# Performance work log

Measured on AMD Instinct MI355X. Metric: run time of the kernel, lower is better.

## Reference

```python
import math
import jax, jax.numpy as jnp
import numpy as np

NHEAD = 4
EPS = 1e-5


def make_pe(max_len, d):
    pos = np.arange(max_len, dtype=np.float32)[:, None]
    div = np.exp(np.arange(0, d, 2, dtype=np.float32) * (-math.log(10000.0) / d))
    pe = np.zeros((max_len, d), np.float32)
    pe[:, 0::2] = np.sin(pos * div)
    pe[:, 1::2] = np.cos(pos * div)
    return jnp.asarray(pe)


def layer_norm(x, g, b):
    m = jnp.mean(x, axis=-1, keepdims=True)
    v = jnp.mean((x - m) ** 2, axis=-1, keepdims=True)
    return (x - m) / jnp.sqrt(v + EPS) * g + b


def mha(q, k, v, wq, bq, wk, bk, wv, bv, wo, bo, kmask=None):
    # q: [b, Lq, d], k/v: [b, Lk, d]
    b_, lq, d = q.shape
    lk = k.shape[1]
    hd = d // NHEAD
    qh = (q @ wq + bq).reshape(b_, lq, NHEAD, hd)
    kh = (k @ wk + bk).reshape(b_, lk, NHEAD, hd)
    vh = (v @ wv + bv).reshape(b_, lk, NHEAD, hd)
    s = jnp.einsum('bqhd,bkhd->bhqk', qh, kh) / jnp.sqrt(jnp.float32(hd))
    if kmask is not None:
        s = jnp.where(kmask[None, None, None, :], s, jnp.float32(-1e9))
    a = jax.nn.softmax(s, axis=-1)
    o = jnp.einsum('bhqk,bkhd->bqhd', a, vh).reshape(b_, lq, d)
    return o @ wo + bo


def _forward(src, in_w, in_b, dec_start,
             e_wq, e_bq, e_wk, e_bk, e_wv, e_bv, e_wo, e_bo,
             e_ln1_g, e_ln1_b, e_w1, e_b1, e_w2, e_b2, e_ln2_g, e_ln2_b,
             d_swq, d_sbq, d_swk, d_sbk, d_swv, d_sbv, d_swo, d_sbo,
             d_ln1_g, d_ln1_b,
             d_cwq, d_cbq, d_cwk, d_cbk, d_cwv, d_cbv, d_cwo, d_cbo,
             d_ln2_g, d_ln2_b,
             d_w1, d_b1, d_w2, d_b2, d_ln3_g, d_ln3_b,
             out_w, out_b, tgt_len):
    B, S = src.shape
    d = in_w.shape[1]
    T = tgt_len
    pe = make_pe(max(S, T) + 10, d)

    # ---- encoder (1 post-norm layer, relu FFN, dropout off) ----
    x = (src[..., None] @ in_w + in_b) * jnp.sqrt(jnp.float32(d))  # [B,S,d]
    x = x + pe[None, :S]
    x = layer_norm(x + mha(x, x, x, e_wq, e_bq, e_wk, e_bk, e_wv, e_bv, e_wo, e_bo), e_ln1_g, e_ln1_b)
    mem = layer_norm(x + (jax.nn.relu(x @ e_w1 + e_b1) @ e_w2 + e_b2), e_ln2_g, e_ln2_b)

    buf0 = jnp.zeros((B, T + 1, d), src.dtype).at[:, 0].set(dec_start[0, 0])
    pe_dec = pe[None, :T + 1]
    kidx = jnp.arange(T + 1)

    def step(buf, t):
        di = buf + pe_dec
        kmask = kidx <= t  # full (non-causal) attention over the t+1 valid tokens
        h = layer_norm(di + mha(di, di, di, d_swq, d_sbq, d_swk, d_sbk,
                                d_swv, d_sbv, d_swo, d_sbo, kmask=kmask),
                       d_ln1_g, d_ln1_b)
        h = layer_norm(h + mha(h, mem, mem, d_cwq, d_cbq, d_cwk, d_cbk,
                               d_cwv, d_cbv, d_cwo, d_cbo),
                       d_ln2_g, d_ln2_b)
        h = layer_norm(h + (jax.nn.relu(h @ d_w1 + d_b1) @ d_w2 + d_b2),
                       d_ln3_g, d_ln3_b)
        last = h[:, t]                       # [B,d] output at the newest position
        buf = buf.at[:, t + 1].set(last)     # feed back as next decoder token
        y = (last @ out_w + out_b)[:, 0]     # [B]
        return buf, y

    _, outs = jax.lax.scan(step, buf0, jnp.arange(T))  # outs: [T,B]
    return outs.T  # [B,T]


def setup_inputs():
    B, S, T, d, ff = 128, 512, 64, 48, 128
    ks = iter(jax.random.split(jax.random.key(0), 64))

    def w(shape, s=0.08):
        return jax.random.normal(next(ks), shape, jnp.float32) * s

    ones = lambda: jnp.ones((d,), jnp.float32)
    zeros = lambda: jnp.zeros((d,), jnp.float32)
    return dict(
        src=jax.random.normal(next(ks), (B, S), jnp.float32),
        in_w=w((1, d)), in_b=w((d,)),
        dec_start=w((1, 1, d), 1.0),
        e_wq=w((d, d)), e_bq=w((d,)), e_wk=w((d, d)), e_bk=w((d,)),
        e_wv=w((d, d)), e_bv=w((d,)), e_wo=w((d, d)), e_bo=w((d,)),
        e_ln1_g=ones(), e_ln1_b=zeros(),
        e_w1=w((d, ff)), e_b1=w((ff,)), e_w2=w((ff, d)), e_b2=w((d,)),
        e_ln2_g=ones(), e_ln2_b=zeros(),
        d_swq=w((d, d)), d_sbq=w((d,)), d_swk=w((d, d)), d_sbk=w((d,)),
        d_swv=w((d, d)), d_sbv=w((d,)), d_swo=w((d, d)), d_sbo=w((d,)),
        d_ln1_g=ones(), d_ln1_b=zeros(),
        d_cwq=w((d, d)), d_cbq=w((d,)), d_cwk=w((d, d)), d_cbk=w((d,)),
        d_cwv=w((d, d)), d_cbv=w((d,)), d_cwo=w((d, d)), d_cbo=w((d,)),
        d_ln2_g=ones(), d_ln2_b=zeros(),
        d_w1=w((d, ff)), d_b1=w((ff,)), d_w2=w((ff, d)), d_b2=w((d,)),
        d_ln3_g=ones(), d_ln3_b=zeros(),
        out_w=w((d, 1)), out_b=w((1,)),
        tgt_len=T,
    )


def reference(src, in_w, in_b, dec_start,
              e_wq, e_bq, e_wk, e_bk, e_wv, e_bv, e_wo, e_bo,
              e_ln1_g, e_ln1_b, e_w1, e_b1, e_w2, e_b2, e_ln2_g, e_ln2_b,
              d_swq, d_sbq, d_swk, d_sbk, d_swv, d_sbv, d_swo, d_sbo,
              d_ln1_g, d_ln1_b,
              d_cwq, d_cbq, d_cwk, d_cbk, d_cwv, d_cbv, d_cwo, d_cbo,
              d_ln2_g, d_ln2_b,
              d_w1, d_b1, d_w2, d_b2, d_ln3_g, d_ln3_b,
              out_w, out_b, tgt_len):
    return _forward(src, in_w, in_b, dec_start,
                    e_wq, e_bq, e_wk, e_bk, e_wv, e_bv, e_wo, e_bo,
                    e_ln1_g, e_ln1_b, e_w1, e_b1, e_w2, e_b2, e_ln2_g, e_ln2_b,
                    d_swq, d_sbq, d_swk, d_sbk, d_swv, d_sbv, d_swo, d_sbo,
                    d_ln1_g, d_ln1_b,
                    d_cwq, d_cbq, d_cwk, d_cbk, d_cwv, d_cbv, d_cwo, d_cbo,
                    d_ln2_g, d_ln2_b,
                    d_w1, d_b1, d_w2, d_b2, d_ln3_g, d_ln3_b,
                    out_w, out_b, tgt_len)
```

## Files before the change

### kernel.cpp

```cpp
#include <hip/hip_runtime.h>
#include <hip/hip_bf16.h>
#include <hip/hip_fp16.h>


constexpr int kB  = 128;
constexpr int kS  = 512;
constexpr int kT  = 64;
constexpr int kD  = 48;
constexpr int kFF = 128;
constexpr int kNH = 4;
constexpr int kHD = 12;

__device__ __forceinline__ void wsync(){
  __builtin_amdgcn_wave_barrier();
  asm volatile("" ::: "memory");
}

__device__ __forceinline__ float wsum(float v){
  #pragma unroll
  for(int o=32;o>=1;o>>=1) v += __shfl_xor(v,o,64);
  return v;
}
__device__ __forceinline__ float wmax(float v){
  #pragma unroll
  for(int o=32;o>=1;o>>=1) v = fmaxf(v,__shfl_xor(v,o,64));
  return v;
}

__device__ __forceinline__ float pe_val(int p, int j){
  int i = j >> 1;
  float f = expf(-0.19188209108283716f * (float)(2*i));
  float a = (float)p * f;
  return (j & 1) ? cosf(a) : sinf(a);
}
__device__ __forceinline__ float pe_fast(int p, int j){
  int i = j >> 1;
  float f = __expf(-0.19188209108283716f * (float)(2*i));
  float a = (float)p * f;
  return (j & 1) ? __cosf(a) : __sinf(a);
}

typedef _Float16 h2v __attribute__((ext_vector_type(2)));
union H2U { __half2 h; h2v v; };
__device__ __forceinline__ float fdot2(__half2 a, __half2 b, float c){
#if __has_builtin(__builtin_amdgcn_fdot2)
  H2U ua, ub; ua.h=a; ub.h=b;
  return __builtin_amdgcn_fdot2(ua.v, ub.v, c, false);
#else
  float2 fa=__half22float2(a), fb=__half22float2(b);
  return fmaf(fa.y, fb.y, fmaf(fa.x, fb.x, c));
#endif
}

__device__ __forceinline__ float dot48d(const __half2* x, const __half* w){
  const __half2* w2=(const __half2*)w;
  float a0=0.f,a1=0.f,a2=0.f,a3=0.f;
  #pragma unroll
  for(int c=0;c<6;c++){
    a0=fdot2(x[4*c+0],w2[4*c+0],a0);
    a1=fdot2(x[4*c+1],w2[4*c+1],a1);
    a2=fdot2(x[4*c+2],w2[4*c+2],a2);
    a3=fdot2(x[4*c+3],w2[4*c+3],a3);
  }
  return (a0+a1)+(a2+a3);
}
__device__ __forceinline__ float dot128d(const __half2* x, const __half* w){
  const __half2* w2=(const __half2*)w;
  float a0=0.f,a1=0.f,a2=0.f,a3=0.f,a4=0.f,a5=0.f,a6=0.f,a7=0.f;
  #pragma unroll
  for(int c=0;c<8;c++){
    a0=fdot2(x[8*c+0],w2[8*c+0],a0);
    a1=fdot2(x[8*c+1],w2[8*c+1],a1);
    a2=fdot2(x[8*c+2],w2[8*c+2],a2);
    a3=fdot2(x[8*c+3],w2[8*c+3],a3);
    a4=fdot2(x[8*c+4],w2[8*c+4],a4);
    a5=fdot2(x[8*c+5],w2[8*c+5],a5);
    a6=fdot2(x[8*c+6],w2[8*c+6],a6);
    a7=fdot2(x[8*c+7],w2[8*c+7],a7);
  }
  return ((a0+a1)+(a2+a3))+((a4+a5)+(a6+a7));
}
__device__ __forceinline__ float dot12f(const float4* x, const float4* k){
  float a=0.f;
  #pragma unroll
  for(int u=0;u<3;u++){ float4 xx=x[u], kk=k[u];
    a+=xx.x*kk.x+xx.y*kk.y+xx.z*kk.z+xx.w*kk.w; }
  return a;
}

__global__ void k_embed(const float* __restrict__ src, const float* __restrict__ in_w,
                        const float* __restrict__ in_b, float* __restrict__ X0){
  int idx = blockIdx.x*256 + threadIdx.x;
  if (idx >= kB*kS*kD) return;
  int j = idx % kD; int bs = idx / kD; int s = bs % kS;
  float v = (src[bs] * in_w[j] + in_b[j]) * 6.928203230275509f;
  X0[idx] = v + pe_fast(s, j);
}

__global__ void __launch_bounds__(256) k_qkv(const float* __restrict__ X,
    const float* __restrict__ wq, const float* __restrict__ bq,
    const float* __restrict__ wk, const float* __restrict__ bk,
    const float* __restrict__ wv, const float* __restrict__ bv,
    __half* __restrict__ Q, __half* __restrict__ K, __half* __restrict__ V){
  __shared__ __align__(16) __half W[3*2688];
  __shared__ __align__(16) float bias[3*kD];
  __shared__ __align__(16) __half2 xt2[32*24];
  int tid = threadIdx.x;
  for (int i=tid;i<3*2304;i+=256){ int m=i/2304, e=i%2304, k=e/48, j=e%48;
    const float* w = (m==0)?wq:((m==1)?wk:wv);
    W[m*2688 + j*56 + k] = __float2half(w[e]); }
  for (int i=tid;i<3*kD;i+=256){ int m=i/kD,e=i%kD;
    const float* w=(m==0)?bq:((m==1)?bk:bv); bias[i]=w[e]; }
  long row0 = (long)blockIdx.x*32;
  const float2* Xp=(const float2*)(X+row0*kD);
  for (int i=tid;i<768;i+=256){ float2 v=Xp[i]; xt2[i]=__floats2half2_rn(v.x,v.y); }
  __syncthreads();
  int r = tid>>3, c0 = tid&7;
  __half2 xr[24];
  #pragma unroll
  for(int u=0;u<24;u++) xr[u]=xt2[r*24+u];
  for (int c=c0; c<3*kD; c+=8){
    int m=c/kD, j=c%kD;
    float acc = bias[m*kD+j] + dot48d(xr, W + m*2688 + j*56);
    __half* o = (m==0)?Q:((m==1)?K:V);
    o[(row0+r)*kD+j]=__float2half(acc);
  }
}

__global__ void __launch_bounds__(256) k_attn(const __half* Q, const __half* __restrict__ K,
                       const __half* __restrict__ V, __half* O){
  int b = blockIdx.x / kNH, h = blockIdx.x % kNH;
  __shared__ __align__(16) __half2 Ks2[kS*6];
  __shared__ __align__(16) float   Vs[kS*kHD];
  int tid = threadIdx.x;
  long base = ((long)b*kS)*kD + h*kHD;
  for (int i=tid;i<kS*6;i+=256){ int r=i/6, c=i%6;
    Ks2[i]=*(const __half2*)&K[base+(long)r*kD+2*c]; }
  for (int i=tid;i<kS*kHD;i+=256){ int r=i/kHD, d=i%kHD;
    Vs[i]=__half2float(V[base+(long)r*kD+d]); }
  const float rs = 0.28867513459481287f;
  int q0 = tid, q1 = tid+256;
  __half2 qa2[6], qb2[6];
  {
    const __half2* qp0=(const __half2*)(Q+base+(long)q0*kD);
    const __half2* qp1=(const __half2*)(Q+base+(long)q1*kD);
    #pragma unroll
    for(int c=0;c<6;c++){ qa2[c]=qp0[c]; qb2[c]=qp1[c]; }
  }
  __syncthreads();
  float acc0[kHD], acc1[kHD];
  #pragma unroll
  for(int j=0;j<kHD;j++){ acc0[j]=0.f; acc1[j]=0.f; }
  float l0=0.f, l1=0.f;
  for(int k=0;k<kS;k++){
    const __half2* kp=Ks2+k*6;
    float sA0=0.f,sA1=0.f,sB0=0.f,sB1=0.f;
    #pragma unroll
    for(int c=0;c<3;c++){
      sA0=fdot2(qa2[2*c],kp[2*c],sA0); sA1=fdot2(qa2[2*c+1],kp[2*c+1],sA1);
      sB0=fdot2(qb2[2*c],kp[2*c],sB0); sB1=fdot2(qb2[2*c+1],kp[2*c+1],sB1);
    }
    float p0=__expf((sA0+sA1)*rs), p1=__expf((sB0+sB1)*rs);
    l0+=p0; l1+=p1;
    const float4* vp=(const float4*)(Vs+k*kHD);
    float4 va=vp[0], vb4=vp[1], vc4=vp[2];
    float vr[kHD]={va.x,va.y,va.z,va.w,vb4.x,vb4.y,vb4.z,vb4.w,vc4.x,vc4.y,vc4.z,vc4.w};
    #pragma unroll
    for(int j=0;j<kHD;j++){ acc0[j]+=p0*vr[j]; acc1[j]+=p1*vr[j]; }
  }
  float i0=1.f/l0, i1=1.f/l1;
  #pragma unroll
  for(int j=0;j<kHD;j++){
    O[base+(long)q0*kD+j]=__float2half(acc0[j]*i0);
    O[base+(long)q1*kD+j]=__float2half(acc1[j]*i1);
  }
}

__global__ void __launch_bounds__(256) k_oproj_ln(const float* __restrict__ Xres, const __half* __restrict__ O,
      const float* __restrict__ wo, const float* __restrict__ bo,
      const float* __restrict__ g, const float* __restrict__ bb,
      __half* __restrict__ Xout){
  __shared__ __align__(16) __half W[kD*56];
  __shared__ float bsh[kD], gs[kD], bs2[kD];
  __shared__ __align__(16) float res[32*kD];
  __shared__ __align__(16) __half2 ot2[32*24];
  __shared__ float mrow[32], rstd[32];
  int tid=threadIdx.x;
  for(int i=tid;i<kD*kD;i+=256){ int k=i/48, j=i%48; W[j*56+k]=__float2half(wo[i]); }
  if(tid<kD){ bsh[tid]=bo[tid]; gs[tid]=g[tid]; bs2[tid]=bb[tid]; }
  long row0=(long)blockIdx.x*32;
  const __half2* Op=(const __half2*)(O+row0*kD);
  for(int i=tid;i<768;i+=256) ot2[i]=Op[i];
  __syncthreads();
  int r=tid>>3, c0=tid&7;
  __half2 orow[24];
  #pragma unroll
  for(int u=0;u<24;u++) orow[u]=ot2[r*24+u];
  for(int j=c0;j<kD;j+=8){
    float acc=bsh[j]+dot48d(orow, W+j*56);
    res[r*kD+j]=Xres[row0*kD + r*kD + j]+acc;
  }
  __syncthreads();
  if(tid<32){
    float s=0.f, s2=0.f;
    for(int j=0;j<kD;j++){ float v=res[tid*kD+j]; s+=v; s2+=v*v; }
    float m=s*(1.f/kD);
    mrow[tid]=m; rstd[tid]=rsqrtf(s2*(1.f/kD)-m*m+1e-5f);
  }
  __syncthreads();
  for(int i=tid;i<32*kD;i+=256){int r2=i/kD,j=i%kD;
    Xout[row0*kD+i]=__float2half((res[i]-mrow[r2])*rstd[r2]*gs[j]+bs2[j]); }
}

__global__ void __launch_bounds__(256) k_ffn_ln(const __half* __restrict__ Xin,
   const float* __restrict__ w1, const float* __restrict__ b1,
   const float* __restrict__ w2, const float* __restrict__ b2,
   const float* __restrict__ g, const float* __restrict__ bb,
   float* __restrict__ Xout){
  __shared__ __align__(16) __half W1[kFF*56];
  __shared__ __align__(16) __half W2[kD*136];
  __shared__ float b1s[kFF], b2s[kD], gs[kD], bs2[kD];
  __shared__ __align__(16) __half xt[16*kD];
  __shared__ __align__(16) __half h1h[16*kFF];
  __shared__ __align__(16) float res[16*kD];
  __shared__ float mrow[16], rstd[16];
  int tid=threadIdx.x;
  for(int i=tid;i<kD*kFF;i+=256){ int k=i/128, c=i%128; W1[c*56+k]=__float2half(w1[i]); }
  for(int i=tid;i<kFF*kD;i+=256){ int u=i/48, j=i%48; W2[j*136+u]=__float2half(w2[i]); }
  if(tid<kFF) b1s[tid]=b1[tid];
  if(tid<kD){ b2s[tid]=b2[tid]; gs[tid]=g[tid]; bs2[tid]=bb[tid]; }
  long row0=(long)blockIdx.x*16;
  const __half2* Xp=(const __half2*)(Xin+row0*kD);
  for(int i=tid;i<384;i+=256) ((__half2*)xt)[i]=Xp[i];
  __syncthreads();
  int r=tid>>4, c0=tid&15;
  {
    __half2 xr[24];
    const __half2* xp=(const __half2*)(xt + r*kD);
    #pragma unroll
    for(int u=0;u<24;u++) xr[u]=xp[u];
    for(int c=c0;c<kFF;c+=16){
      float acc=b1s[c]+dot48d(xr, W1+c*56);
      h1h[r*kFF+c]=__float2half(fmaxf(acc,0.f));
    }
  }
  __syncthreads();
  {
    const __half2* hp=(const __half2*)(h1h + r*kFF);
    for(int j=c0;j<kD;j+=16){
      float acc=b2s[j]+dot128d(hp, W2+j*136);
      res[r*kD+j]=__half2float(xt[r*kD+j])+acc;
    }
  }
  __syncthreads();
  if(tid<16){
    float s=0.f, s2=0.f;
    for(int j=0;j<kD;j++){ float v=res[tid*kD+j]; s+=v; s2+=v*v; }
    float m=s*(1.f/kD);
    mrow[tid]=m; rstd[tid]=rsqrtf(s2*(1.f/kD)-m*m+1e-5f);
  }
  __syncthreads();
  for(int i=tid;i<16*kD;i+=256){int r2=i/kD,j=i%kD;
    Xout[row0*kD+i]=(res[i]-mrow[r2])*rstd[r2]*gs[j]+bs2[j]; }
}

__global__ void __launch_bounds__(256) k_ckv(const float* __restrict__ M,
    const float* __restrict__ wk, const float* __restrict__ bk,
    const float* __restrict__ wv, const float* __restrict__ bv,
    __half* __restrict__ Kc, __half* __restrict__ Vc){
  __shared__ __align__(16) __half W[2*2688];
  __shared__ float bias[2*kD];
  __shared__ __align__(16) __half2 xt2[32*24];
  int tid=threadIdx.x;
  for(int i=tid;i<2*2304;i+=256){ int m=i/2304, e=i%2304, k=e/48, j=e%48;
    W[m*2688 + j*56 + k] = __float2half((m?wv:wk)[e]); }
  for(int i=tid;i<2*kD;i+=256){ int m=i/kD,e=i%kD; bias[i]=(m?bv:bk)[e]; }
  long row0=(long)blockIdx.x*32;
  const float2* Mp=(const float2*)(M+row0*kD);
  for(int i=tid;i<768;i+=256){ float2 v=Mp[i]; xt2[i]=__floats2half2_rn(v.x,v.y); }
  __syncthreads();
  int r=tid>>3, c0=tid&7;
  __half2 xr[24];
  #pragma unroll
  for(int u=0;u<24;u++) xr[u]=xt2[r*24+u];
  long gr=row0+r; long bb2=gr>>9; long s=gr&511;
  for(int c=c0;c<2*kD;c+=8){
    int m=c/kD, j=c%kD;
    float acc=bias[m*kD+j]+dot48d(xr, W+m*2688+j*56);
    if(m==0) Kc[(bb2*kS+s)*kD + j]=__float2half(acc);
    else     Vc[(bb2*kD+j)*kS + s]=__float2half(acc);
  }
}

__global__ void k_prep(const float* __restrict__ swq,const float* __restrict__ swk,
                       const float* __restrict__ swv,const float* __restrict__ swo,
                       const float* __restrict__ cwq,const float* __restrict__ cwo,
                       const float* __restrict__ w1,const float* __restrict__ w2,
                       __half* __restrict__ Wh){
  int idx=blockIdx.x*256+threadIdx.x;
  if(idx>=26112) return;
  if(idx<13824){
    int m=idx/2304, e=idx%2304, j=e/48, k=e%48;
    const float* w = (m==0)?swq:((m==1)?swk:((m==2)?swv:((m==3)?swo:((m==4)?cwq:cwo))));
    Wh[m*2688 + j*56 + k] = __float2half(w[k*48+j]);
  } else if(idx<19968){
    int e=idx-13824, c=e/48, k=e%48;
    Wh[16128 + c*56 + k] = __float2half(w1[k*128+c]);
  } else {
    int e=idx-19968, j=e/128, u=e%128;
    Wh[23296 + j*136 + u] = __float2half(w2[u*48+j]);
  }
}

struct DecP {
  const float *dec_start, *sbq, *sbk, *sbv, *sbo, *ln1g, *ln1b,
              *cbq, *cbo, *ln2g, *ln2b, *fb1, *fb2, *ln3g, *ln3b, *ow, *ob;
};

__global__ void __launch_bounds__(256,1) k_dec(const __half* __restrict__ KT,
    const __half* __restrict__ VT, const __half* __restrict__ Wg, DecP P,
    float* __restrict__ out){
  __shared__ __align__(16) __half Wl[29824];
  __shared__ __align__(16) float Kh[kNH*kT*kHD];
  __shared__ __align__(16) float Vh[kNH*kT*kHD];
  __shared__ __align__(16) float qS[kNH*16];
  __shared__ __align__(16) __half xvH[kD], soH[kD], h1H[kD], cqH[kD], covH[kD], h2H[kD];
  __shared__ __align__(16) __half f1H[kFF];
  __shared__ __align__(16) float peT[kT*kD];
  int tid=threadIdx.x, b=blockIdx.x, wave=tid>>6, lane=tid&63;
  const float rs=0.28867513459481287f;

  for(int i=tid;i<29824/8;i+=256) ((float4*)Wl)[i]=((const float4*)Wg)[i];
  for(int i=tid;i<kT*kD;i+=256){ int tt=i/kD, j=i%kD; peT[i]=pe_val(tt,j); }

  float cur=0, c_bo=0,c_cbq=0,c_cbo=0,c_fb2=0;
  float g1=0,bb1=0,g2=0,bb2=0,g3=0,bb3=0,c_ow=0;
  if(wave==0 && lane<kD){
    cur=P.dec_start[lane];
    c_bo=P.sbo[lane]; c_cbq=P.cbq[lane]; c_cbo=P.cbo[lane]; c_fb2=P.fb2[lane];
    g1=P.ln1g[lane]; bb1=P.ln1b[lane];
    g2=P.ln2g[lane]; bb2=P.ln2b[lane];
    g3=P.ln3g[lane]; bb3=P.ln3b[lane];
    c_ow=P.ow[lane];
  }
  float c_qkvb=0;
  if(wave>=1 && lane<kD)
    c_qkvb = ((wave==1)?P.sbq:((wave==2)?P.sbk:P.sbv))[lane];
  float c_fb1=0;
  if(wave<2) c_fb1=P.fb1[wave*64+lane];
  float c_ob=P.ob[0];

  __half2 Kr2[4][2][6], Vr2[4][kHD];
  {
    const __half* Kb = KT + (long)b*kS*kD;
    const __half2* Vb = (const __half2*)VT + (long)b*kD*(kS/2);
    #pragma unroll
    for(int i=0;i<4;i++){
      int sp = lane + 64*i;
      #pragma unroll
      for(int e=0;e<2;e++){
        const __half2* kp=(const __half2*)(Kb + (long)(2*sp+e)*kD + wave*kHD);
        #pragma unroll
        for(int c=0;c<6;c++) Kr2[i][e][c]=kp[c];
      }
      #pragma unroll
      for(int u=0;u<kHD;u++) Vr2[i][u]=Vb[(wave*kHD+u)*(kS/2)+sp];
    }
  }
  __syncthreads();

  float h1=0, h2=0, xv=0;
  for(int t=0;t<kT;t++){
    if(wave==0 && lane<kD){ xv=cur+peT[t*kD+lane]; xvH[lane]=__float2half(xv); }
    __syncthreads();
    if(wave>=1 && lane<kD){
      int m=wave-1;
      float a=c_qkvb+dot48d((const __half2*)xvH, Wl + m*2688 + lane*56);
      int hh=lane/kHD, dd=lane%kHD;
      if(m==0) qS[hh*16+dd]=a;
      else if(m==1) Kh[(hh*kT+t)*kHD+dd]=a;
      else          Vh[(hh*kT+t)*kHD+dd]=a;
    }
    __syncthreads();
    {
      float p=0.f, pv[kHD];
      #pragma unroll
      for(int u=0;u<kHD;u++) pv[u]=0.f;
      if(lane<=t){
        float s=dot12f((const float4*)(qS+wave*16),
                       (const float4*)(Kh+(wave*kT+lane)*kHD))*rs;
        p=__expf(s);
        const float4* vp=(const float4*)(Vh+(wave*kT+lane)*kHD);
        float4 v0=vp[0], v1=vp[1], v2=vp[2];
        float vr[kHD]={v0.x,v0.y,v0.z,v0.w,v1.x,v1.y,v1.z,v1.w,v2.x,v2.y,v2.z,v2.w};
        #pragma unroll
        for(int u=0;u<kHD;u++) pv[u]=p*vr[u];
      }
      float l=wsum(p);
      #pragma unroll
      for(int u=0;u<kHD;u++) pv[u]=wsum(pv[u]);
      if(lane==0){
        float inv=1.f/l;
        #pragma unroll
        for(int u=0;u<6;u++)
          ((__half2*)soH)[wave*6+u]=__floats2half2_rn(pv[2*u]*inv, pv[2*u+1]*inv);
      }
    }
    __syncthreads();
    if(wave==0){
      float rr=0.f;
      if(lane<kD)
        rr=xv+c_bo+dot48d((const __half2*)soH, Wl+8064+lane*56);
      float s1=wsum(rr), s2=wsum(rr*rr);
      float mean=s1*(1.f/48.f);
      float rstd=rsqrtf(s2*(1.f/48.f)-mean*mean+1e-5f);
      h1=0;
      if(lane<kD){ h1=(rr-mean)*rstd*g1+bb1; h1H[lane]=__float2half(h1); }
      wsync();
      if(lane<kD)
        cqH[lane]=__float2half(c_cbq+dot48d((const __half2*)h1H, Wl+10752+lane*56));
    }
    __syncthreads();
    {
      __half2 q2[6];
      #pragma unroll
      for(int c=0;c<6;c++) q2[c]=((const __half2*)cqH)[wave*6+c];
      float s[8];
      #pragma unroll
      for(int i=0;i<4;i++){
        #pragma unroll
        for(int e=0;e<2;e++){
          float a0=0.f,a1=0.f;
          const __half2* kp=Kr2[i][e];
          a0=fdot2(q2[0],kp[0],a0); a1=fdot2(q2[1],kp[1],a1);
          a0=fdot2(q2[2],kp[2],a0); a1=fdot2(q2[3],kp[3],a1);
          a0=fdot2(q2[4],kp[4],a0); a1=fdot2(q2[5],kp[5],a1);
          s[2*i+e]=(a0+a1)*rs;
        }
      }
      float mloc=s[0];
      #pragma unroll
      for(int j=1;j<8;j++) mloc=fmaxf(mloc,s[j]);
      float M=wmax(mloc);
      float p[8], l=0.f;
      #pragma unroll
      for(int j=0;j<8;j++){ p[j]=__expf(s[j]-M); l+=p[j]; }
      l=wsum(l);
      float inv=1.f/l;
      __half2 ph[4];
      #pragma unroll
      for(int i=0;i<4;i++) ph[i]=__floats2half2_rn(p[2*i],p[2*i+1]);
      float acc[kHD];
      #pragma unroll
      for(int u=0;u<kHD;u++) acc[u]=0.f;
      #pragma unroll
      for(int i=0;i<4;i++){
        #pragma unroll
        for(int u=0;u<kHD;u++) acc[u]=fdot2(ph[i],Vr2[i][u],acc[u]);
      }
      #pragma unroll
      for(int u=0;u<kHD;u++) acc[u]=wsum(acc[u]);
      if(lane==0){
        #pragma unroll
        for(int u=0;u<6;u++)
          ((__half2*)covH)[wave*6+u]=__floats2half2_rn(acc[2*u]*inv, acc[2*u+1]*inv);
      }
    }
    __syncthreads();
    if(wave==0){
      float rr=0.f;
      if(lane<kD)
        rr=h1+c_cbo+dot48d((const __half2*)covH, Wl+13440+lane*56);
      float s1=wsum(rr), s2=wsum(rr*rr);
      float mean=s1*(1.f/48.f);
      float rstd=rsqrtf(s2*(1.f/48.f)-mean*mean+1e-5f);
      h2=0;
      if(lane<kD){ h2=(rr-mean)*rstd*g2+bb2; h2H[lane]=__float2half(h2); }
    }
    __syncthreads();
    if(wave<2){
      int col=wave*64+lane;
      float a=c_fb1+dot48d((const __half2*)h2H, Wl+16128+col*56);
      f1H[col]=__float2half(fmaxf(a,0.f));
    }
    __syncthreads();
    if(wave==0){
      float rr=0.f;
      if(lane<kD)
        rr=h2+c_fb2+dot128d((const __half2*)f1H, Wl+23296+lane*136);
      float s1=wsum(rr), s2=wsum(rr*rr);
      float mean=s1*(1.f/48.f);
      float rstd=rsqrtf(s2*(1.f/48.f)-mean*mean+1e-5f);
      float cv=0.f;
      if(lane<kD){ cv=(rr-mean)*rstd*g3+bb3; cur=cv; }
      float y=wsum(cv*c_ow);
      if(lane==0) out[b*kT+t]=y+c_ob;
    }
  }
}

extern "C" void kernel_launch(void* const* d_in, const int* in_sizes, int n_in,
                              void* d_out, int out_size, void* d_ws, size_t ws_size,
                              hipStream_t stream){
  float* ws = (float*)d_ws;
  __half* Wh = (__half*)ws;
  const size_t NB = (size_t)kB*kS*kD;
  float*  A  = ws + 16384;
  __half* H1 = (__half*)(A + NB);
  __half* H2 = H1 + NB;
  __half* H3 = H2 + NB;

  k_embed<<<(kB*kS*kD+255)/256,256,0,stream>>>((const float*)d_in[0],(const float*)d_in[1],(const float*)d_in[2],A);
  k_qkv  <<<(kB*kS)/32,256,0,stream>>>(A,(const float*)d_in[4],(const float*)d_in[5],(const float*)d_in[6],
                                       (const float*)d_in[7],(const float*)d_in[8],(const float*)d_in[9],H1,H2,H3);
  k_attn <<<kB*kNH,256,0,stream>>>(H1,H2,H3,H1);
  k_oproj_ln<<<(kB*kS)/32,256,0,stream>>>(A,H1,(const float*)d_in[10],(const float*)d_in[11],
                                          (const float*)d_in[12],(const float*)d_in[13],H2);
  k_ffn_ln  <<<(kB*kS)/16,256,0,stream>>>(H2,(const float*)d_in[14],(const float*)d_in[15],(const float*)d_in[16],
                                          (const float*)d_in[17],(const float*)d_in[18],(const float*)d_in[19],A);
  k_ckv     <<<(kB*kS)/32,256,0,stream>>>(A,(const float*)d_in[32],(const float*)d_in[33],
                                          (const float*)d_in[34],(const float*)d_in[35],H1,H3);
  k_prep    <<<(26112+255)/256,256,0,stream>>>((const float*)d_in[20],(const float*)d_in[22],(const float*)d_in[24],
                                               (const float*)d_in[26],(const float*)d_in[30],(const float*)d_in[36],
                                               (const float*)d_in[40],(const float*)d_in[42],Wh);
  DecP P;
  P.dec_start=(const float*)d_in[3];
  P.sbq=(const float*)d_in[21]; P.sbk=(const float*)d_in[23]; P.sbv=(const float*)d_in[25]; P.sbo=(const float*)d_in[27];
  P.ln1g=(const float*)d_in[28]; P.ln1b=(const float*)d_in[29];
  P.cbq=(const float*)d_in[31]; P.cbo=(const float*)d_in[37];
  P.ln2g=(const float*)d_in[38]; P.ln2b=(const float*)d_in[39];
  P.fb1=(const float*)d_in[41]; P.fb2=(const float*)d_in[43];
  P.ln3g=(const float*)d_in[44]; P.ln3b=(const float*)d_in[45];
  P.ow=(const float*)d_in[46]; P.ob=(const float*)d_in[47];
  k_dec<<<kB,256,0,stream>>>(H1,H3,Wh,P,(float*)d_out);
}
```

Before: 688.5 us.

## Pack two decode batches per block and use DPP wave reductions

The decoder kernel now runs two independent batch chains per 512-thread block. Both chains share one LDS copy of the weights and positional table, and the per-chain scratch buffers are doubled. This halves the block count and the weight staging per batch, but the two chains now synchronize together at every barrier. Wave reductions move from shfl_xor to DPP row operations plus a readlane, which is meant to cut the latency of each reduction in the serial decode chain.

```diff
diff --git a/kernel.cpp b/kernel.cpp
--- a/kernel.cpp
+++ b/kernel.cpp
@@ -16,15 +16,29 @@
   asm volatile("" ::: "memory");
 }
 
-__device__ __forceinline__ float wsum(float v){
-  #pragma unroll
-  for(int o=32;o>=1;o>>=1) v += __shfl_xor(v,o,64);
-  return v;
-}
-__device__ __forceinline__ float wmax(float v){
-  #pragma unroll
-  for(int o=32;o>=1;o>>=1) v = fmaxf(v,__shfl_xor(v,o,64));
-  return v;
+template<int CTRL,int RM,int BM,bool BC>
+__device__ __forceinline__ float dppmov(float x, float old){
+  return __builtin_bit_cast(float, __builtin_amdgcn_update_dpp(
+      __builtin_bit_cast(int, old), __builtin_bit_cast(int, x), CTRL, RM, BM, BC));
+}
+__device__ __forceinline__ float wsum(float x){
+  x += dppmov<0x111,0xf,0xf,true>(x, 0.f);
+  x += dppmov<0x112,0xf,0xf,true>(x, 0.f);
+  x += dppmov<0x114,0xf,0xf,true>(x, 0.f);
+  x += dppmov<0x118,0xf,0xf,true>(x, 0.f);
+  x += dppmov<0x142,0xa,0xf,true>(x, 0.f);
+  x += dppmov<0x143,0xc,0xf,true>(x, 0.f);
+  return __builtin_bit_cast(float, __builtin_amdgcn_readlane(__builtin_bit_cast(int, x), 63));
+}
+__device__ __forceinline__ float wmax(float x){
+  const float NI = -3.4e38f;
+  x = fmaxf(x, dppmov<0x111,0xf,0xf,false>(x, NI));
+  x = fmaxf(x, dppmov<0x112,0xf,0xf,false>(x, NI));
+  x = fmaxf(x, dppmov<0x114,0xf,0xf,false>(x, NI));
+  x = fmaxf(x, dppmov<0x118,0xf,0xf,false>(x, NI));
+  x = fmaxf(x, dppmov<0x142,0xa,0xf,false>(x, NI));
+  x = fmaxf(x, dppmov<0x143,0xc,0xf,false>(x, NI));
+  return __builtin_bit_cast(float, __builtin_amdgcn_readlane(__builtin_bit_cast(int, x), 63));
 }
 
 __device__ __forceinline__ float pe_val(int p, int j){
@@ -317,21 +331,24 @@
               *cbq, *cbo, *ln2g, *ln2b, *fb1, *fb2, *ln3g, *ln3b, *ow, *ob;
 };
 
-__global__ void __launch_bounds__(256,1) k_dec(const __half* __restrict__ KT,
+__global__ void __launch_bounds__(512,1) k_dec(const __half* __restrict__ KT,
     const __half* __restrict__ VT, const __half* __restrict__ Wg, DecP P,
     float* __restrict__ out){
   __shared__ __align__(16) __half Wl[29824];
-  __shared__ __align__(16) float Kh[kNH*kT*kHD];
-  __shared__ __align__(16) float Vh[kNH*kT*kHD];
-  __shared__ __align__(16) float qS[kNH*16];
-  __shared__ __align__(16) __half xvH[kD], soH[kD], h1H[kD], cqH[kD], covH[kD], h2H[kD];
-  __shared__ __align__(16) __half f1H[kFF];
   __shared__ __align__(16) float peT[kT*kD];
-  int tid=threadIdx.x, b=blockIdx.x, wave=tid>>6, lane=tid&63;
+  __shared__ __align__(16) float Kh[2][kNH*kT*kHD];
+  __shared__ __align__(16) float Vh[2][kNH*kT*kHD];
+  __shared__ __align__(16) float qS[2][kNH*16];
+  __shared__ __align__(16) __half xvH[2][kD], soH[2][kD], h1H[2][kD],
+                                  cqH[2][kD], covH[2][kD], h2H[2][kD];
+  __shared__ __align__(16) __half f1H[2][kFF];
+  int tid=threadIdx.x;
+  int chain = tid>>8, ctid = tid&255, wave=ctid>>6, lane=ctid&63;
+  int b = blockIdx.x*2 + chain;
   const float rs=0.28867513459481287f;
 
-  for(int i=tid;i<29824/8;i+=256) ((float4*)Wl)[i]=((const float4*)Wg)[i];
-  for(int i=tid;i<kT*kD;i+=256){ int tt=i/kD, j=i%kD; peT[i]=pe_val(tt,j); }
+  for(int i=tid;i<29824/8;i+=512) ((float4*)Wl)[i]=((const float4*)Wg)[i];
+  for(int i=tid;i<kT*kD;i+=512){ int tt=i/kD, j=i%kD; peT[i]=pe_val(tt,j); }
 
   float cur=0, c_bo=0,c_cbq=0,c_cbo=0,c_fb2=0;
   float g1=0,bb1=0,g2=0,bb2=0,g3=0,bb3=0,c_ow=0;
@@ -371,15 +388,15 @@
 
   float h1=0, h2=0, xv=0;
   for(int t=0;t<kT;t++){
-    if(wave==0 && lane<kD){ xv=cur+peT[t*kD+lane]; xvH[lane]=__float2half(xv); }
+    if(wave==0 && lane<kD){ xv=cur+peT[t*kD+lane]; xvH[chain][lane]=__float2half(xv); }
     __syncthreads();
     if(wave>=1 && lane<kD){
       int m=wave-1;
-      float a=c_qkvb+dot48d((const __half2*)xvH, Wl + m*2688 + lane*56);
+      float a=c_qkvb+dot48d((const __half2*)xvH[chain], Wl + m*2688 + lane*56);
       int hh=lane/kHD, dd=lane%kHD;
-      if(m==0) qS[hh*16+dd]=a;
-      else if(m==1) Kh[(hh*kT+t)*kHD+dd]=a;
-      else          Vh[(hh*kT+t)*kHD+dd]=a;
+      if(m==0) qS[chain][hh*16+dd]=a;
+      else if(m==1) Kh[chain][(hh*kT+t)*kHD+dd]=a;
+      else          Vh[chain][(hh*kT+t)*kHD+dd]=a;
     }
     __syncthreads();
     {
@@ -387,10 +404,10 @@
       #pragma unroll
       for(int u=0;u<kHD;u++) pv[u]=0.f;
       if(lane<=t){
-        float s=dot12f((const float4*)(qS+wave*16),
-                       (const float4*)(Kh+(wave*kT+lane)*kHD))*rs;
+        float s=dot12f((const float4*)(qS[chain]+wave*16),
+                       (const float4*)(Kh[chain]+(wave*kT+lane)*kHD))*rs;
         p=__expf(s);
-        const float4* vp=(const float4*)(Vh+(wave*kT+lane)*kHD);
+        const float4* vp=(const float4*)(Vh[chain]+(wave*kT+lane)*kHD);
         float4 v0=vp[0], v1=vp[1], v2=vp[2];
         float vr[kHD]={v0.x,v0.y,v0.z,v0.w,v1.x,v1.y,v1.z,v1.w,v2.x,v2.y,v2.z,v2.w};
         #pragma unroll
@@ -403,28 +420,28 @@
         float inv=1.f/l;
         #pragma unroll
         for(int u=0;u<6;u++)
-          ((__half2*)soH)[wave*6+u]=__floats2half2_rn(pv[2*u]*inv, pv[2*u+1]*inv);
+          ((__half2*)soH[chain])[wave*6+u]=__floats2half2_rn(pv[2*u]*inv, pv[2*u+1]*inv);
       }
     }
     __syncthreads();
     if(wave==0){
       float rr=0.f;
       if(lane<kD)
-        rr=xv+c_bo+dot48d((const __half2*)soH, Wl+8064+lane*56);
+        rr=xv+c_bo+dot48d((const __half2*)soH[chain], Wl+8064+lane*56);
       float s1=wsum(rr), s2=wsum(rr*rr);
       float mean=s1*(1.f/48.f);
       float rstd=rsqrtf(s2*(1.f/48.f)-mean*mean+1e-5f);
       h1=0;
-      if(lane<kD){ h1=(rr-mean)*rstd*g1+bb1; h1H[lane]=__float2half(h1); }
+      if(lane<kD){ h1=(rr-mean)*rstd*g1+bb1; h1H[chain][lane]=__float2half(h1); }
       wsync();
       if(lane<kD)
-        cqH[lane]=__float2half(c_cbq+dot48d((const __half2*)h1H, Wl+10752+lane*56));
+        cqH[chain][lane]=__float2half(c_cbq+dot48d((const __half2*)h1H[chain], Wl+10752+lane*56));
     }
     __syncthreads();
     {
       __half2 q2[6];
       #pragma unroll
-      for(int c=0;c<6;c++) q2[c]=((const __half2*)cqH)[wave*6+c];
+      for(int c=0;c<6;c++) q2[c]=((const __half2*)cqH[chain])[wave*6+c];
       float s[8];
       #pragma unroll
       for(int i=0;i<4;i++){
@@ -463,31 +480,31 @@
       if(lane==0){
         #pragma unroll
         for(int u=0;u<6;u++)
-          ((__half2*)covH)[wave*6+u]=__floats2half2_rn(acc[2*u]*inv, acc[2*u+1]*inv);
+          ((__half2*)covH[chain])[wave*6+u]=__floats2half2_rn(acc[2*u]*inv, acc[2*u+1]*inv);
       }
     }
     __syncthreads();
     if(wave==0){
       float rr=0.f;
       if(lane<kD)
-        rr=h1+c_cbo+dot48d((const __half2*)covH, Wl+13440+lane*56);
+        rr=h1+c_cbo+dot48d((const __half2*)covH[chain], Wl+13440+lane*56);
       float s1=wsum(rr), s2=wsum(rr*rr);
       float mean=s1*(1.f/48.f);
       float rstd=rsqrtf(s2*(1.f/48.f)-mean*mean+1e-5f);
       h2=0;
-      if(lane<kD){ h2=(rr-mean)*rstd*g2+bb2; h2H[lane]=__float2half(h2); }
+      if(lane<kD){ h2=(rr-mean)*rstd*g2+bb2; h2H[chain][lane]=__float2half(h2); }
     }
     __syncthreads();
     if(wave<2){
       int col=wave*64+lane;
-      float a=c_fb1+dot48d((const __half2*)h2H, Wl+16128+col*56);
-      f1H[col]=__float2half(fmaxf(a,0.f));
+      float a=c_fb1+dot48d((const __half2*)h2H[chain], Wl+16128+col*56);
+      f1H[chain][col]=__float2half(fmaxf(a,0.f));
     }
     __syncthreads();
     if(wave==0){
       float rr=0.f;
       if(lane<kD)
-        rr=h2+c_fb2+dot128d((const __half2*)f1H, Wl+23296+lane*136);
+        rr=h2+c_fb2+dot128d((const __half2*)f1H[chain], Wl+23296+lane*136);
       float s1=wsum(rr), s2=wsum(rr*rr);
       float mean=s1*(1.f/48.f);
       float rstd=rsqrtf(s2*(1.f/48.f)-mean*mean+1e-5f);
@@ -532,5 +549,5 @@
   P.fb1=(const float*)d_in[41]; P.fb2=(const float*)d_in[43];
   P.ln3g=(const float*)d_in[44]; P.ln3b=(const float*)d_in[45];
   P.ow=(const float*)d_in[46]; P.ob=(const float*)d_in[47];
-  k_dec<<<kB,256,0,stream>>>(H1,H3,Wh,P,(float*)d_out);
-}
+  k_dec<<<kB/2,512,0,stream>>>(H1,H3,Wh,P,(float*)d_out);
+}
```

Result: faster. 671.7 us (-2.4%).

## Run decoder serial stages in one wave and use DPP reductions

Applied to the files above, without the earlier changes.

Moves the self-attention QKV projection, the self-attention over cached keys, and the FFN first layer into wave 0. Those stages were split across waves with block barriers between them and now run under wave-level syncs only. This removes several __syncthreads per decode step. Self-attention now splits keys into 16-lane groups per head and reduces with DPP row sums. Wave reductions switch from shuffle-xor to DPP row ops plus readlane, and self-attention K is stored in half precision. The trade is less parallelism in those stages in exchange for fewer barriers and cheaper reductions.

```diff
diff --git a/kernel.cpp b/kernel.cpp
--- a/kernel.cpp
+++ b/kernel.cpp
@@ -16,15 +16,36 @@
   asm volatile("" ::: "memory");
 }
 
-__device__ __forceinline__ float wsum(float v){
-  #pragma unroll
-  for(int o=32;o>=1;o>>=1) v += __shfl_xor(v,o,64);
-  return v;
-}
-__device__ __forceinline__ float wmax(float v){
-  #pragma unroll
-  for(int o=32;o>=1;o>>=1) v = fmaxf(v,__shfl_xor(v,o,64));
-  return v;
+template<int CTRL,int RM,int BM,bool BC>
+__device__ __forceinline__ float dppmov(float x, float old){
+  return __builtin_bit_cast(float, __builtin_amdgcn_update_dpp(
+      __builtin_bit_cast(int, old), __builtin_bit_cast(int, x), CTRL, RM, BM, BC));
+}
+__device__ __forceinline__ float wsum(float x){
+  x += dppmov<0x111,0xf,0xf,true>(x, 0.f);
+  x += dppmov<0x112,0xf,0xf,true>(x, 0.f);
+  x += dppmov<0x114,0xf,0xf,true>(x, 0.f);
+  x += dppmov<0x118,0xf,0xf,true>(x, 0.f);
+  x += dppmov<0x142,0xa,0xf,true>(x, 0.f);
+  x += dppmov<0x143,0xc,0xf,true>(x, 0.f);
+  return __builtin_bit_cast(float, __builtin_amdgcn_readlane(__builtin_bit_cast(int, x), 63));
+}
+__device__ __forceinline__ float wmax(float x){
+  const float NI = -3.4e38f;
+  x = fmaxf(x, dppmov<0x111,0xf,0xf,false>(x, NI));
+  x = fmaxf(x, dppmov<0x112,0xf,0xf,false>(x, NI));
+  x = fmaxf(x, dppmov<0x114,0xf,0xf,false>(x, NI));
+  x = fmaxf(x, dppmov<0x118,0xf,0xf,false>(x, NI));
+  x = fmaxf(x, dppmov<0x142,0xa,0xf,false>(x, NI));
+  x = fmaxf(x, dppmov<0x143,0xc,0xf,false>(x, NI));
+  return __builtin_bit_cast(float, __builtin_amdgcn_readlane(__builtin_bit_cast(int, x), 63));
+}
+__device__ __forceinline__ float rowsum16(float x){
+  x += dppmov<0x111,0xf,0xf,true>(x, 0.f);
+  x += dppmov<0x112,0xf,0xf,true>(x, 0.f);
+  x += dppmov<0x114,0xf,0xf,true>(x, 0.f);
+  x += dppmov<0x118,0xf,0xf,true>(x, 0.f);
+  return x;
 }
 
 __device__ __forceinline__ float pe_val(int p, int j){
@@ -79,13 +100,6 @@
     a7=fdot2(x[8*c+7],w2[8*c+7],a7);
   }
   return ((a0+a1)+(a2+a3))+((a4+a5)+(a6+a7));
-}
-__device__ __forceinline__ float dot12f(const float4* x, const float4* k){
-  float a=0.f;
-  #pragma unroll
-  for(int u=0;u<3;u++){ float4 xx=x[u], kk=k[u];
-    a+=xx.x*kk.x+xx.y*kk.y+xx.z*kk.z+xx.w*kk.w; }
-  return a;
 }
 
 __global__ void k_embed(const float* __restrict__ src, const float* __restrict__ in_w,
@@ -321,33 +335,32 @@
     const __half* __restrict__ VT, const __half* __restrict__ Wg, DecP P,
     float* __restrict__ out){
   __shared__ __align__(16) __half Wl[29824];
-  __shared__ __align__(16) float Kh[kNH*kT*kHD];
-  __shared__ __align__(16) float Vh[kNH*kT*kHD];
-  __shared__ __align__(16) float qS[kNH*16];
+  __shared__ __align__(16) float peT[kT*kD];
+  __shared__ __align__(16) __half KhH[kNH*kT*kHD];
+  __shared__ __align__(16) float  Vh[kNH*kT*kHD];
+  __shared__ __align__(16) __half qSH[kNH*kHD];
   __shared__ __align__(16) __half xvH[kD], soH[kD], h1H[kD], cqH[kD], covH[kD], h2H[kD];
   __shared__ __align__(16) __half f1H[kFF];
-  __shared__ __align__(16) float peT[kT*kD];
   int tid=threadIdx.x, b=blockIdx.x, wave=tid>>6, lane=tid&63;
   const float rs=0.28867513459481287f;
 
   for(int i=tid;i<29824/8;i+=256) ((float4*)Wl)[i]=((const float4*)Wg)[i];
   for(int i=tid;i<kT*kD;i+=256){ int tt=i/kD, j=i%kD; peT[i]=pe_val(tt,j); }
 
-  float cur=0, c_bo=0,c_cbq=0,c_cbo=0,c_fb2=0;
-  float g1=0,bb1=0,g2=0,bb2=0,g3=0,bb3=0,c_ow=0;
-  if(wave==0 && lane<kD){
-    cur=P.dec_start[lane];
-    c_bo=P.sbo[lane]; c_cbq=P.cbq[lane]; c_cbo=P.cbo[lane]; c_fb2=P.fb2[lane];
-    g1=P.ln1g[lane]; bb1=P.ln1b[lane];
-    g2=P.ln2g[lane]; bb2=P.ln2b[lane];
-    g3=P.ln3g[lane]; bb3=P.ln3b[lane];
-    c_ow=P.ow[lane];
-  }
-  float c_qkvb=0;
-  if(wave>=1 && lane<kD)
-    c_qkvb = ((wave==1)?P.sbq:((wave==2)?P.sbk:P.sbv))[lane];
-  float c_fb1=0;
-  if(wave<2) c_fb1=P.fb1[wave*64+lane];
+  float cur=0, c_sbq=0,c_sbk=0,c_sbv=0, c_bo=0,c_cbq=0,c_cbo=0,c_fb2=0;
+  float g1=0,bb1=0,g2=0,bb2=0,g3=0,bb3=0,c_ow=0, c_fb1a=0,c_fb1b=0;
+  if(wave==0){
+    if(lane<kD){
+      cur=P.dec_start[lane];
+      c_sbq=P.sbq[lane]; c_sbk=P.sbk[lane]; c_sbv=P.sbv[lane];
+      c_bo=P.sbo[lane]; c_cbq=P.cbq[lane]; c_cbo=P.cbo[lane]; c_fb2=P.fb2[lane];
+      g1=P.ln1g[lane]; bb1=P.ln1b[lane];
+      g2=P.ln2g[lane]; bb2=P.ln2b[lane];
+      g3=P.ln3g[lane]; bb3=P.ln3b[lane];
+      c_ow=P.ow[lane];
+    }
+    c_fb1a=P.fb1[lane]; c_fb1b=P.fb1[lane+64];
+  }
   float c_ob=P.ob[0];
 
   __half2 Kr2[4][2][6], Vr2[4][kHD];
@@ -371,51 +384,67 @@
 
   float h1=0, h2=0, xv=0;
   for(int t=0;t<kT;t++){
-    if(wave==0 && lane<kD){ xv=cur+peT[t*kD+lane]; xvH[lane]=__float2half(xv); }
-    __syncthreads();
-    if(wave>=1 && lane<kD){
-      int m=wave-1;
-      float a=c_qkvb+dot48d((const __half2*)xvH, Wl + m*2688 + lane*56);
-      int hh=lane/kHD, dd=lane%kHD;
-      if(m==0) qS[hh*16+dd]=a;
-      else if(m==1) Kh[(hh*kT+t)*kHD+dd]=a;
-      else          Vh[(hh*kT+t)*kHD+dd]=a;
-    }
-    __syncthreads();
-    {
-      float p=0.f, pv[kHD];
-      #pragma unroll
-      for(int u=0;u<kHD;u++) pv[u]=0.f;
-      if(lane<=t){
-        float s=dot12f((const float4*)(qS+wave*16),
-                       (const float4*)(Kh+(wave*kT+lane)*kHD))*rs;
-        p=__expf(s);
-        const float4* vp=(const float4*)(Vh+(wave*kT+lane)*kHD);
-        float4 v0=vp[0], v1=vp[1], v2=vp[2];
-        float vr[kHD]={v0.x,v0.y,v0.z,v0.w,v1.x,v1.y,v1.z,v1.w,v2.x,v2.y,v2.z,v2.w};
-        #pragma unroll
-        for(int u=0;u<kHD;u++) pv[u]=p*vr[u];
-      }
-      float l=wsum(p);
-      #pragma unroll
-      for(int u=0;u<kHD;u++) pv[u]=wsum(pv[u]);
-      if(lane==0){
-        float inv=1.f/l;
-        #pragma unroll
-        for(int u=0;u<6;u++)
-          ((__half2*)soH)[wave*6+u]=__floats2half2_rn(pv[2*u]*inv, pv[2*u+1]*inv);
-      }
-    }
-    __syncthreads();
     if(wave==0){
-      float rr=0.f;
-      if(lane<kD)
-        rr=xv+c_bo+dot48d((const __half2*)soH, Wl+8064+lane*56);
-      float s1=wsum(rr), s2=wsum(rr*rr);
-      float mean=s1*(1.f/48.f);
-      float rstd=rsqrtf(s2*(1.f/48.f)-mean*mean+1e-5f);
-      h1=0;
-      if(lane<kD){ h1=(rr-mean)*rstd*g1+bb1; h1H[lane]=__float2half(h1); }
+      if(lane<kD){ xv=cur+peT[t*kD+lane]; xvH[lane]=__float2half(xv); }
+      wsync();
+      if(lane<kD){
+        float qv=c_sbq+dot48d((const __half2*)xvH, Wl + 0*2688 + lane*56);
+        float kv=c_sbk+dot48d((const __half2*)xvH, Wl + 1*2688 + lane*56);
+        float vv=c_sbv+dot48d((const __half2*)xvH, Wl + 2*2688 + lane*56);
+        int hh=lane/kHD, dd=lane%kHD;
+        qSH[lane]=__float2half(qv);
+        KhH[(hh*kT+t)*kHD+dd]=__float2half(kv);
+        Vh[(hh*kT+t)*kHD+dd]=vv;
+      }
+      wsync();
+      {
+        int hh=lane>>4, g=lane&15;
+        __half2 q2[6];
+        const __half2* qp=(const __half2*)qSH + hh*6;
+        #pragma unroll
+        for(int c=0;c<6;c++) q2[c]=qp[c];
+        float l=0.f, acc[kHD];
+        #pragma unroll
+        for(int u=0;u<kHD;u++) acc[u]=0.f;
+        #pragma unroll
+        for(int kk=0;kk<4;kk++){
+          int key=g+16*kk;
+          if(key<=t){
+            const __half2* kp=(const __half2*)KhH + (hh*kT+key)*6;
+            float a0=0.f,a1=0.f;
+            a0=fdot2(q2[0],kp[0],a0); a1=fdot2(q2[1],kp[1],a1);
+            a0=fdot2(q2[2],kp[2],a0); a1=fdot2(q2[3],kp[3],a1);
+            a0=fdot2(q2[4],kp[4],a0); a1=fdot2(q2[5],kp[5],a1);
+            float p=__expf((a0+a1)*rs);
+            l+=p;
+            const float4* vp=(const float4*)(Vh+(hh*kT+key)*kHD);
+            float4 v0=vp[0], v1=vp[1], v2=vp[2];
+            float vr[kHD]={v0.x,v0.y,v0.z,v0.w,v1.x,v1.y,v1.z,v1.w,v2.x,v2.y,v2.z,v2.w};
+            #pragma unroll
+            for(int u=0;u<kHD;u++) acc[u]+=p*vr[u];
+          }
+        }
+        l=rowsum16(l);
+        #pragma unroll
+        for(int u=0;u<kHD;u++) acc[u]=rowsum16(acc[u]);
+        if(g==15){
+          float inv=1.f/l;
+          #pragma unroll
+          for(int u=0;u<6;u++)
+            ((__half2*)soH)[hh*6+u]=__floats2half2_rn(acc[2*u]*inv, acc[2*u+1]*inv);
+        }
+      }
+      wsync();
+      {
+        float rr=0.f;
+        if(lane<kD)
+          rr=xv+c_bo+dot48d((const __half2*)soH, Wl+8064+lane*56);
+        float s1=wsum(rr), s2=wsum(rr*rr);
+        float mean=s1*(1.f/48.f);
+        float rstd=rsqrtf(s2*(1.f/48.f)-mean*mean+1e-5f);
+        h1=0;
+        if(lane<kD){ h1=(rr-mean)*rstd*g1+bb1; h1H[lane]=__float2half(h1); }
+      }
       wsync();
       if(lane<kD)
         cqH[lane]=__float2half(c_cbq+dot48d((const __half2*)h1H, Wl+10752+lane*56));
@@ -468,33 +497,36 @@
     }
     __syncthreads();
     if(wave==0){
-      float rr=0.f;
-      if(lane<kD)
-        rr=h1+c_cbo+dot48d((const __half2*)covH, Wl+13440+lane*56);
-      float s1=wsum(rr), s2=wsum(rr*rr);
-      float mean=s1*(1.f/48.f);
-      float rstd=rsqrtf(s2*(1.f/48.f)-mean*mean+1e-5f);
-      h2=0;
-      if(lane<kD){ h2=(rr-mean)*rstd*g2+bb2; h2H[lane]=__float2half(h2); }
-    }
-    __syncthreads();
-    if(wave<2){
-      int col=wave*64+lane;
-      float a=c_fb1+dot48d((const __half2*)h2H, Wl+16128+col*56);
-      f1H[col]=__float2half(fmaxf(a,0.f));
-    }
-    __syncthreads();
-    if(wave==0){
-      float rr=0.f;
-      if(lane<kD)
-        rr=h2+c_fb2+dot128d((const __half2*)f1H, Wl+23296+lane*136);
-      float s1=wsum(rr), s2=wsum(rr*rr);
-      float mean=s1*(1.f/48.f);
-      float rstd=rsqrtf(s2*(1.f/48.f)-mean*mean+1e-5f);
-      float cv=0.f;
-      if(lane<kD){ cv=(rr-mean)*rstd*g3+bb3; cur=cv; }
-      float y=wsum(cv*c_ow);
-      if(lane==0) out[b*kT+t]=y+c_ob;
+      {
+        float rr=0.f;
+        if(lane<kD)
+          rr=h1+c_cbo+dot48d((const __half2*)covH, Wl+13440+lane*56);
+        float s1=wsum(rr), s2=wsum(rr*rr);
+        float mean=s1*(1.f/48.f);
+        float rstd=rsqrtf(s2*(1.f/48.f)-mean*mean+1e-5f);
+        h2=0;
+        if(lane<kD){ h2=(rr-mean)*rstd*g2+bb2; h2H[lane]=__float2half(h2); }
+      }
+      wsync();
+      {
+        float a=c_fb1a+dot48d((const __half2*)h2H, Wl+16128+lane*56);
+        float bcol=c_fb1b+dot48d((const __half2*)h2H, Wl+16128+(lane+64)*56);
+        f1H[lane]=__float2half(fmaxf(a,0.f));
+        f1H[lane+64]=__float2half(fmaxf(bcol,0.f));
+      }
+      wsync();
+      {
+        float rr=0.f;
+        if(lane<kD)
+          rr=h2+c_fb2+dot128d((const __half2*)f1H, Wl+23296+lane*136);
+        float s1=wsum(rr), s2=wsum(rr*rr);
+        float mean=s1*(1.f/48.f);
+        float rstd=rsqrtf(s2*(1.f/48.f)-mean*mean+1e-5f);
+        float cv=0.f;
+        if(lane<kD){ cv=(rr-mean)*rstd*g3+bb3; cur=cv; }
+        float y=wsum(cv*c_ow);
+        if(lane==0) out[b*kT+t]=y+c_ob;
+      }
     }
   }
 }
```

Result: faster. 589.3 us (-14.4%).
